# Optimization experiments

Measured on AMD Instinct MI355X. Metric: run time of the kernel, lower is better.

Reference implementation:

```python
import jax, jax.numpy as jnp
import numpy as np

N_QUBITS = 10   # log2(32*32)
N_LAYERS = 5
GRID = 32


def _u3_gates(weights):
    # weights: [L, Q, 3] float32 -> gates: [L, Q, 2, 2] complex64
    th, ph, lm = weights[..., 0], weights[..., 1], weights[..., 2]
    cos = jnp.cos(th / 2)
    sin = jnp.sin(th / 2)
    u00 = cos.astype(jnp.complex64)
    u01 = -jnp.exp(1j * lm) * sin
    u10 = jnp.exp(1j * ph) * sin
    u11 = jnp.exp(1j * (ph + lm)) * cos
    row0 = jnp.stack([u00, u01], axis=-1)
    row1 = jnp.stack([u10, u11], axis=-1)
    return jnp.stack([row0, row1], axis=-2)


def _build_unitary(weights):
    N = 1 << N_QUBITS
    gates = _u3_gates(weights)
    # U as tensor [N, 2, 2, ..., 2]; axis q+1 is qubit q's column index
    U = jnp.eye(N, dtype=jnp.complex64).reshape((N,) + (2,) * N_QUBITS)
    for l in range(N_LAYERS):
        # single-qubit U3 rotations
        for q in range(N_QUBITS):
            ax = q + 1
            s = jnp.moveaxis(U, ax, -1)
            s = jnp.einsum('...a,ba->...b', s, gates[l, q])
            U = jnp.moveaxis(s, -1, ax)
        # circular CNOTs: control q -> target (q+1) % N_QUBITS
        for q in range(N_QUBITS):
            c_ax = q + 1
            t_ax = ((q + 1) % N_QUBITS) + 1
            s = jnp.moveaxis(U, (c_ax, t_ax), (-2, -1))
            # when control bit == 1, flip target bit (swap the two target slices)
            s = s.at[..., 1, :].set(s[..., 1, ::-1])
            U = jnp.moveaxis(s, (-2, -1), (c_ax, t_ax))
    return U.reshape(N, N)


def setup_inputs() -> dict:
    key = jax.random.key(0)
    k1, k2 = jax.random.split(key)
    x_freq = jax.random.normal(k1, (128, 16, GRID, GRID), dtype=jnp.float32)
    weights = jax.random.normal(k2, (N_LAYERS, N_QUBITS, 3), dtype=jnp.float32) * 0.1
    return {"x_freq": x_freq, "weights": weights}


def reference(x_freq, weights):
    B, C, H, W = x_freq.shape
    state = x_freq.reshape(B, C, -1).astype(jnp.complex64)  # [B, C, N]
    U = _build_unitary(weights)                              # [N, N]
    out = jnp.einsum('ij,bcj->bci', U, state)
    return out.reshape(B, C, H, W)
```

## Files before the change

kernel.cpp:

```cpp
#include <hip/hip_runtime.h>


#define NQ 10
#define NL 5
#define NST 1024
#define NTH 64

typedef float f2 __attribute__((ext_vector_type(2)));

constexpr int csigma(int i) {
  for (int q = 0; q < NQ; ++q) {
    const int cb = 9 - q, tb = 9 - ((q + 1) % NQ);
    i ^= ((i >> cb) & 1) << tb;
  }
  return i;
}

__device__ __forceinline__ int swz(int k) { return k ^ (((k >> 4) & 7) << 1); }

__global__ void build_gates(const float* __restrict__ w, float* __restrict__ gw) {
  const int t = threadIdx.x;
  if (t < NL * NQ) {
    const float th = w[t * 3 + 0], ph = w[t * 3 + 1], lm = w[t * 3 + 2];
    const float ch = cosf(0.5f * th), sh = sinf(0.5f * th);
    const float cl = cosf(lm), sl = sinf(lm);
    const float cp = cosf(ph), sp = sinf(ph);
    const float cpl = cosf(ph + lm), spl = sinf(ph + lm);
    float* G = gw + t * 8;
    G[0] = ch;       G[1] = 0.0f;
    G[2] = cp * sh;  G[3] = sp * sh;
    G[4] = -cl * sh; G[5] = -sl * sh;
    G[6] = cpl * ch; G[7] = spl * ch;
  }
}

__device__ __forceinline__ void bfly(f2& a, f2& b, const float h00,
                                     const float h01x, const float h01y,
                                     const float h10x, const float h10y,
                                     const float h11x, const float h11y) {
  const f2 ia = (f2){-a.y, a.x};
  const f2 ib = (f2){-b.y, b.x};
  const f2 na = h00 * a + h01x * b + h01y * ib;
  const f2 nb = h10x * a + h10y * ia + h11x * b + h11y * ib;
  a = na;
  b = nb;
}

#define LOAD_G(G)                                             \
  const float h00 = (G)[0];                                   \
  const float h01x = (G)[2], h01y = (G)[3];                   \
  const float h10x = (G)[4], h10y = (G)[5];                   \
  const float h11x = (G)[6], h11y = (G)[7];

__global__ __launch_bounds__(NTH) void qc_apply(
    const float* __restrict__ x, const float* __restrict__ gw,
    float* __restrict__ out, int out_size) {
  __shared__ alignas(16) f2 sc[NST];

  const int t = threadIdx.x;
  const int sv = blockIdx.x;
  const int m = (t & 7) << 1;

  {
    const float* xs = x + (size_t)sv * NST;
#pragma unroll
    for (int jp = 0; jp < 4; ++jp) {
      const float4 xv = ((const float4*)xs)[t * 4 + jp];
      const int j0 = (jp * 4) ^ m;
      *(float4*)&sc[(t << 4) | j0]       = make_float4(xv.x, 0.f, xv.y, 0.f);
      *(float4*)&sc[(t << 4) | (j0 ^ 2)] = make_float4(xv.z, 0.f, xv.w, 0.f);
    }
  }
  __syncthreads();

  int sL = t;
#pragma unroll
  for (int q = 0; q < NQ; ++q) {
    const int cb = 9 - q, tb = 9 - ((q + 1) % NQ);
    sL ^= ((sL >> cb) & 1) << tb;
  }
  constexpr int SH6 = csigma(1 << 6), SH7 = csigma(1 << 7),
                SH8 = csigma(1 << 8), SH9 = csigma(1 << 9);

  f2 v[16];

#pragma unroll 1
  for (int l = NL - 1; l >= 0; --l) {
    const float* gl = gw + l * NQ * 8;

#pragma unroll
    for (int r = 0; r < 16; ++r) {
      const int idx = sL ^ ((r & 1) ? SH6 : 0) ^ ((r & 2) ? SH7 : 0) ^
                      ((r & 4) ? SH8 : 0) ^ ((r & 8) ? SH9 : 0);
      v[r] = sc[swz(idx)];
    }
#pragma unroll
    for (int e = 0; e < 4; ++e) {
      LOAD_G(gl + (3 - e) * 8)
#pragma unroll
      for (int r = 0; r < 16; ++r)
        if (!(r & (1 << e)))
          bfly(v[r], v[r | (1 << e)], h00, h01x, h01y, h10x, h10y, h11x, h11y);
    }
    __syncthreads();
#pragma unroll
    for (int r = 0; r < 16; ++r) sc[swz((r << 6) | t)] = v[r];
    __syncthreads();

    const int cbase = ((t >> 4) << 8) | (t & 15);
#pragma unroll
    for (int r = 0; r < 16; ++r) v[r] = sc[swz(cbase | (r << 4))];
#pragma unroll
    for (int e = 0; e < 2; ++e) {
      LOAD_G(gl + (5 - e) * 8)
#pragma unroll
      for (int r = 0; r < 16; ++r)
        if (!(r & (1 << e)))
          bfly(v[r], v[r | (1 << e)], h00, h01x, h01y, h10x, h10y, h11x, h11y);
    }
    __syncthreads();
#pragma unroll
    for (int r = 0; r < 16; ++r) sc[swz(cbase | (r << 4))] = v[r];
    __syncthreads();

#pragma unroll
    for (int rp = 0; rp < 8; ++rp) {
      const float4 p = *(const float4*)&sc[(t << 4) | ((2 * rp) ^ m)];
      v[2 * rp]     = (f2){p.x, p.y};
      v[2 * rp + 1] = (f2){p.z, p.w};
    }
#pragma unroll
    for (int e = 0; e < 4; ++e) {
      LOAD_G(gl + (9 - e) * 8)
#pragma unroll
      for (int r = 0; r < 16; ++r)
        if (!(r & (1 << e)))
          bfly(v[r], v[r | (1 << e)], h00, h01x, h01y, h10x, h10y, h11x, h11y);
    }
    if (l != 0) {
#pragma unroll
      for (int rp = 0; rp < 8; ++rp) {
        *(float4*)&sc[(t << 4) | ((2 * rp) ^ m)] =
            make_float4(v[2 * rp].x, v[2 * rp].y,
                        v[2 * rp + 1].x, v[2 * rp + 1].y);
      }
      __syncthreads();
    }
  }

  const size_t ob = (size_t)sv * NST + (t << 4);
#pragma unroll
  for (int rp = 0; rp < 4; ++rp) {
    if (ob + 4 * rp + 4 <= (size_t)out_size)
      *(float4*)(out + ob + 4 * rp) =
          make_float4(v[4 * rp].x, v[4 * rp + 1].x,
                      v[4 * rp + 2].x, v[4 * rp + 3].x);
  }
}

extern "C" void kernel_launch(void* const* d_in, const int* in_sizes, int n_in,
                              void* d_out, int out_size, void* d_ws, size_t ws_size,
                              hipStream_t stream) {
  const float* x = (const float*)d_in[0];
  const float* w = (const float*)d_in[1];
  float* out = (float*)d_out;
  float* gw = (float*)d_ws;
  const int nstates = in_sizes[0] / NST;
  build_gates<<<1, 64, 0, stream>>>(w, gw);
  qc_apply<<<nstates, NTH, 0, stream>>>(x, gw, out, out_size);
}
```

Before: 85.01 us.

## Use 128 threads per state with 8 amplitudes each and shuffle for one qubit

Doubles the threads per state-vector block from 64 to 128, so each thread holds 8 amplitudes instead of 16. The qubit passes are regrouped into three 3-qubit register passes. The tenth qubit (gate index 5) is handled with a cross-lane xor-2 shuffle instead of another shared-memory round trip, which removes one LDS exchange and its barriers per layer. The LDS swizzle is redefined to avoid bank conflicts under the new access patterns. The aim is higher occupancy and latency hiding with lower register pressure, in exchange for more threads and shuffle traffic.

```diff
diff --git a/kernel.cpp b/kernel.cpp
--- a/kernel.cpp
+++ b/kernel.cpp
@@ -4,7 +4,7 @@
 #define NQ 10
 #define NL 5
 #define NST 1024
-#define NTH 64
+#define NTH 128
 
 typedef float f2 __attribute__((ext_vector_type(2)));
 
@@ -16,7 +16,9 @@
   return i;
 }
 
-__device__ __forceinline__ int swz(int k) { return k ^ (((k >> 4) & 7) << 1); }
+__device__ __forceinline__ int swz(int k) {
+  return k ^ ((((k >> 4) ^ (k >> 7)) & 7) << 1);
+}
 
 __global__ void build_gates(const float* __restrict__ w, float* __restrict__ gw) {
   const int t = threadIdx.x;
@@ -59,17 +61,16 @@
 
   const int t = threadIdx.x;
   const int sv = blockIdx.x;
-  const int m = (t & 7) << 1;
+  const int mT = (((t >> 1) ^ (t >> 4)) & 7) << 1;
 
   {
     const float* xs = x + (size_t)sv * NST;
-#pragma unroll
-    for (int jp = 0; jp < 4; ++jp) {
-      const float4 xv = ((const float4*)xs)[t * 4 + jp];
-      const int j0 = (jp * 4) ^ m;
-      *(float4*)&sc[(t << 4) | j0]       = make_float4(xv.x, 0.f, xv.y, 0.f);
-      *(float4*)&sc[(t << 4) | (j0 ^ 2)] = make_float4(xv.z, 0.f, xv.w, 0.f);
-    }
+    const float4 x0 = ((const float4*)xs)[2 * t];
+    const float4 x1 = ((const float4*)xs)[2 * t + 1];
+    *(float4*)&sc[(8 * t + 0) ^ mT] = make_float4(x0.x, 0.f, x0.y, 0.f);
+    *(float4*)&sc[(8 * t + 2) ^ mT] = make_float4(x0.z, 0.f, x0.w, 0.f);
+    *(float4*)&sc[(8 * t + 4) ^ mT] = make_float4(x1.x, 0.f, x1.y, 0.f);
+    *(float4*)&sc[(8 * t + 6) ^ mT] = make_float4(x1.z, 0.f, x1.w, 0.f);
   }
   __syncthreads();
 
@@ -79,82 +80,104 @@
     const int cb = 9 - q, tb = 9 - ((q + 1) % NQ);
     sL ^= ((sL >> cb) & 1) << tb;
   }
-  constexpr int SH6 = csigma(1 << 6), SH7 = csigma(1 << 7),
-                SH8 = csigma(1 << 8), SH9 = csigma(1 << 9);
+  constexpr int SH7 = csigma(1 << 7), SH8 = csigma(1 << 8),
+                SH9 = csigma(1 << 9);
 
-  f2 v[16];
+  f2 v[8];
 
 #pragma unroll 1
   for (int l = NL - 1; l >= 0; --l) {
     const float* gl = gw + l * NQ * 8;
 
 #pragma unroll
-    for (int r = 0; r < 16; ++r) {
-      const int idx = sL ^ ((r & 1) ? SH6 : 0) ^ ((r & 2) ? SH7 : 0) ^
-                      ((r & 4) ? SH8 : 0) ^ ((r & 8) ? SH9 : 0);
+    for (int r = 0; r < 8; ++r) {
+      const int idx = sL ^ ((r & 1) ? SH7 : 0) ^ ((r & 2) ? SH8 : 0) ^
+                      ((r & 4) ? SH9 : 0);
       v[r] = sc[swz(idx)];
     }
 #pragma unroll
-    for (int e = 0; e < 4; ++e) {
-      LOAD_G(gl + (3 - e) * 8)
+    for (int e = 0; e < 3; ++e) {
+      LOAD_G(gl + (2 - e) * 8)
 #pragma unroll
-      for (int r = 0; r < 16; ++r)
+      for (int r = 0; r < 8; ++r)
         if (!(r & (1 << e)))
           bfly(v[r], v[r | (1 << e)], h00, h01x, h01y, h10x, h10y, h11x, h11y);
     }
     __syncthreads();
 #pragma unroll
-    for (int r = 0; r < 16; ++r) sc[swz((r << 6) | t)] = v[r];
+    for (int r = 0; r < 8; ++r) sc[swz((r << 7) | t)] = v[r];
     __syncthreads();
 
-    const int cbase = ((t >> 4) << 8) | (t & 15);
+    const int bbase = (t & 7) | (((t >> 3) & 1) << 4) | ((t >> 4) << 7);
 #pragma unroll
-    for (int r = 0; r < 16; ++r) v[r] = sc[swz(cbase | (r << 4))];
+    for (int r = 0; r < 8; ++r) {
+      const int idx = bbase | ((r & 1) << 3) | (((r >> 1) & 1) << 5) |
+                      (((r >> 2) & 1) << 6);
+      v[r] = sc[swz(idx)];
+    }
+    {
+      const int GQ[3] = {6, 4, 3};
 #pragma unroll
-    for (int e = 0; e < 2; ++e) {
-      LOAD_G(gl + (5 - e) * 8)
+      for (int e = 0; e < 3; ++e) {
+        LOAD_G(gl + GQ[e] * 8)
 #pragma unroll
-      for (int r = 0; r < 16; ++r)
+        for (int r = 0; r < 8; ++r)
+          if (!(r & (1 << e)))
+            bfly(v[r], v[r | (1 << e)], h00, h01x, h01y, h10x, h10y, h11x, h11y);
+      }
+    }
+#pragma unroll
+    for (int r = 0; r < 8; ++r) {
+      const int idx = bbase | ((r & 1) << 3) | (((r >> 1) & 1) << 5) |
+                      (((r >> 2) & 1) << 6);
+      sc[swz(idx)] = v[r];
+    }
+    __syncthreads();
+
+#pragma unroll
+    for (int j0 = 0; j0 < 8; j0 += 2) {
+      const float4 p = *(const float4*)&sc[(8 * t + j0) ^ mT];
+      v[j0]     = (f2){p.x, p.y};
+      v[j0 + 1] = (f2){p.z, p.w};
+    }
+#pragma unroll
+    for (int e = 0; e < 3; ++e) {
+      LOAD_G(gl + (9 - e) * 8)
+#pragma unroll
+      for (int r = 0; r < 8; ++r)
         if (!(r & (1 << e)))
           bfly(v[r], v[r | (1 << e)], h00, h01x, h01y, h10x, h10y, h11x, h11y);
     }
-    __syncthreads();
+    {
+      LOAD_G(gl + 5 * 8)
+      const bool hi = (t >> 1) & 1;
+      const float c1 = hi ? h11x : h00;
+      const float c2 = hi ? h11y : 0.0f;
+      const float c3 = hi ? h10x : h01x;
+      const float c4 = hi ? h10y : h01y;
 #pragma unroll
-    for (int r = 0; r < 16; ++r) sc[swz(cbase | (r << 4))] = v[r];
-    __syncthreads();
-
-#pragma unroll
-    for (int rp = 0; rp < 8; ++rp) {
-      const float4 p = *(const float4*)&sc[(t << 4) | ((2 * rp) ^ m)];
-      v[2 * rp]     = (f2){p.x, p.y};
-      v[2 * rp + 1] = (f2){p.z, p.w};
-    }
-#pragma unroll
-    for (int e = 0; e < 4; ++e) {
-      LOAD_G(gl + (9 - e) * 8)
-#pragma unroll
-      for (int r = 0; r < 16; ++r)
-        if (!(r & (1 << e)))
-          bfly(v[r], v[r | (1 << e)], h00, h01x, h01y, h10x, h10y, h11x, h11y);
+      for (int r = 0; r < 8; ++r) {
+        f2 p;
+        p.x = __shfl_xor(v[r].x, 2);
+        p.y = __shfl_xor(v[r].y, 2);
+        const f2 iv = (f2){-v[r].y, v[r].x};
+        const f2 ip = (f2){-p.y, p.x};
+        v[r] = c1 * v[r] + c2 * iv + c3 * p + c4 * ip;
+      }
     }
     if (l != 0) {
 #pragma unroll
-      for (int rp = 0; rp < 8; ++rp) {
-        *(float4*)&sc[(t << 4) | ((2 * rp) ^ m)] =
-            make_float4(v[2 * rp].x, v[2 * rp].y,
-                        v[2 * rp + 1].x, v[2 * rp + 1].y);
-      }
+      for (int j0 = 0; j0 < 8; j0 += 2)
+        *(float4*)&sc[(8 * t + j0) ^ mT] =
+            make_float4(v[j0].x, v[j0].y, v[j0 + 1].x, v[j0 + 1].y);
       __syncthreads();
     }
   }
 
-  const size_t ob = (size_t)sv * NST + (t << 4);
-#pragma unroll
-  for (int rp = 0; rp < 4; ++rp) {
-    if (ob + 4 * rp + 4 <= (size_t)out_size)
-      *(float4*)(out + ob + 4 * rp) =
-          make_float4(v[4 * rp].x, v[4 * rp + 1].x,
-                      v[4 * rp + 2].x, v[4 * rp + 3].x);
+  const size_t ob = (size_t)sv * NST + 8 * t;
+  if (ob + 8 <= (size_t)out_size) {
+    *(float4*)(out + ob)     = make_float4(v[0].x, v[1].x, v[2].x, v[3].x);
+    *(float4*)(out + ob + 4) = make_float4(v[4].x, v[5].x, v[6].x, v[7].x);
   }
 }
 
```

New measurement: 85.33 us. Within noise of the previous version (+0.4%).

## Rebalance qubit passes to 4/4/2 with new shared-memory layout and swizzle

Applied to the files above, without the earlier changes.

Reorganizes the per-layer qubit grouping so the three shared-memory passes handle 4, 4 and 2 qubits instead of 4, 2 and 4. It introduces a permuted storage layout (rawA) and a new XOR swizzle with precomputed read offsets, so that the permuted reads and writes avoid bank conflicts. The output write is also reshaped so each thread stores coalesced float4 chunks spread across four 256-element segments. The outer layer loop is no longer forced to stay rolled, and the final pass now adds an extra barrier before writing back. The vectorized float4 shared-memory accesses are replaced by scalar f2 ones.

```diff
diff --git a/kernel.cpp b/kernel.cpp
--- a/kernel.cpp
+++ b/kernel.cpp
@@ -16,7 +16,18 @@
   return i;
 }
 
-__device__ __forceinline__ int swz(int k) { return k ^ (((k >> 4) & 7) << 1); }
+constexpr int cswz(int p) { return p ^ ((((p >> 4) ^ (p >> 7)) & 7) << 1); }
+constexpr int crawA(int j) {
+  return (((j >> 2) & 63) << 4) | (j & 3) | (((j >> 8) & 3) << 2);
+}
+constexpr int SRv(int r) { return cswz(crawA(csigma(r << 6))); }
+
+__device__ __forceinline__ int swz(int p) {
+  return p ^ ((((p >> 4) ^ (p >> 7)) & 7) << 1);
+}
+__device__ __forceinline__ int rawA(int j) {
+  return (((j >> 2) & 63) << 4) | (j & 3) | (((j >> 8) & 3) << 2);
+}
 
 __global__ void build_gates(const float* __restrict__ w, float* __restrict__ gw) {
   const int t = threadIdx.x;
@@ -59,41 +70,45 @@
 
   const int t = threadIdx.x;
   const int sv = blockIdx.x;
-  const int m = (t & 7) << 1;
 
   {
     const float* xs = x + (size_t)sv * NST;
 #pragma unroll
-    for (int jp = 0; jp < 4; ++jp) {
-      const float4 xv = ((const float4*)xs)[t * 4 + jp];
-      const int j0 = (jp * 4) ^ m;
-      *(float4*)&sc[(t << 4) | j0]       = make_float4(xv.x, 0.f, xv.y, 0.f);
-      *(float4*)&sc[(t << 4) | (j0 ^ 2)] = make_float4(xv.z, 0.f, xv.w, 0.f);
+    for (int i4 = 0; i4 < 4; ++i4) {
+      const float4 xv = ((const float4*)xs)[4 * t + i4];
+      const int k = 16 * t + 4 * i4;
+      const int pa = swz(rawA(k));
+      *(float4*)&sc[pa]     = make_float4(xv.x, 0.f, xv.y, 0.f);
+      *(float4*)&sc[pa ^ 2] = make_float4(xv.z, 0.f, xv.w, 0.f);
     }
   }
   __syncthreads();
 
-  int sL = t;
+  int st = t;
 #pragma unroll
   for (int q = 0; q < NQ; ++q) {
     const int cb = 9 - q, tb = 9 - ((q + 1) % NQ);
-    sL ^= ((sL >> cb) & 1) << tb;
+    st ^= ((st >> cb) & 1) << tb;
   }
-  constexpr int SH6 = csigma(1 << 6), SH7 = csigma(1 << 7),
-                SH8 = csigma(1 << 8), SH9 = csigma(1 << 9);
+  const int A0 = swz(rawA(st));
+  static constexpr int SR[16] = {
+      SRv(0),  SRv(1),  SRv(2),  SRv(3),  SRv(4),  SRv(5),  SRv(6),  SRv(7),
+      SRv(8),  SRv(9),  SRv(10), SRv(11), SRv(12), SRv(13), SRv(14), SRv(15)};
+
+  const int WB = ((t & 3) << 4) | ((t >> 2) & 15);
+  const int RB = (((t >> 2) & 15) << 6) | ((t & 3) << 4);
+  const int j69 = (t >> 2) & 15;
+  const int WC = ((j69 & 3) << 8) | (t & 3) | (((j69 >> 2) & 3) << 2);
+  const int RC = (((t >> 4) & 3) << 8) | ((t & 15) << 4);
+  const int WA = t << 4;
 
   f2 v[16];
 
-#pragma unroll 1
   for (int l = NL - 1; l >= 0; --l) {
     const float* gl = gw + l * NQ * 8;
 
 #pragma unroll
-    for (int r = 0; r < 16; ++r) {
-      const int idx = sL ^ ((r & 1) ? SH6 : 0) ^ ((r & 2) ? SH7 : 0) ^
-                      ((r & 4) ? SH8 : 0) ^ ((r & 8) ? SH9 : 0);
-      v[r] = sc[swz(idx)];
-    }
+    for (int r = 0; r < 16; ++r) v[r] = sc[A0 ^ SR[r]];
 #pragma unroll
     for (int e = 0; e < 4; ++e) {
       LOAD_G(gl + (3 - e) * 8)
@@ -104,15 +119,14 @@
     }
     __syncthreads();
 #pragma unroll
-    for (int r = 0; r < 16; ++r) sc[swz((r << 6) | t)] = v[r];
+    for (int r = 0; r < 16; ++r) sc[swz(WB | (r << 6))] = v[r];
     __syncthreads();
 
-    const int cbase = ((t >> 4) << 8) | (t & 15);
 #pragma unroll
-    for (int r = 0; r < 16; ++r) v[r] = sc[swz(cbase | (r << 4))];
+    for (int r = 0; r < 16; ++r) v[r] = sc[swz(RB | r)];
 #pragma unroll
-    for (int e = 0; e < 2; ++e) {
-      LOAD_G(gl + (5 - e) * 8)
+    for (int e = 0; e < 4; ++e) {
+      LOAD_G(gl + (7 - e) * 8)
 #pragma unroll
       for (int r = 0; r < 16; ++r)
         if (!(r & (1 << e)))
@@ -120,41 +134,40 @@
     }
     __syncthreads();
 #pragma unroll
-    for (int r = 0; r < 16; ++r) sc[swz(cbase | (r << 4))] = v[r];
+    for (int r = 0; r < 16; ++r) sc[swz(WC | (r << 4))] = v[r];
     __syncthreads();
 
 #pragma unroll
-    for (int rp = 0; rp < 8; ++rp) {
-      const float4 p = *(const float4*)&sc[(t << 4) | ((2 * rp) ^ m)];
-      v[2 * rp]     = (f2){p.x, p.y};
-      v[2 * rp + 1] = (f2){p.z, p.w};
-    }
-#pragma unroll
-    for (int e = 0; e < 4; ++e) {
-      LOAD_G(gl + (9 - e) * 8)
+    for (int r = 0; r < 16; ++r) v[r] = sc[swz(RC | r)];
+    {
+      LOAD_G(gl + 9 * 8)
 #pragma unroll
       for (int r = 0; r < 16; ++r)
-        if (!(r & (1 << e)))
-          bfly(v[r], v[r | (1 << e)], h00, h01x, h01y, h10x, h10y, h11x, h11y);
+        if (!(r & 1))
+          bfly(v[r], v[r | 1], h00, h01x, h01y, h10x, h10y, h11x, h11y);
+    }
+    {
+      LOAD_G(gl + 8 * 8)
+#pragma unroll
+      for (int r = 0; r < 16; ++r)
+        if (!(r & 2))
+          bfly(v[r], v[r | 2], h00, h01x, h01y, h10x, h10y, h11x, h11y);
     }
     if (l != 0) {
+      __syncthreads();
 #pragma unroll
-      for (int rp = 0; rp < 8; ++rp) {
-        *(float4*)&sc[(t << 4) | ((2 * rp) ^ m)] =
-            make_float4(v[2 * rp].x, v[2 * rp].y,
-                        v[2 * rp + 1].x, v[2 * rp + 1].y);
-      }
+      for (int r = 0; r < 16; ++r) sc[swz(WA | r)] = v[r];
       __syncthreads();
     }
   }
 
-  const size_t ob = (size_t)sv * NST + (t << 4);
+  const size_t ob = (size_t)sv * NST;
 #pragma unroll
-  for (int rp = 0; rp < 4; ++rp) {
-    if (ob + 4 * rp + 4 <= (size_t)out_size)
-      *(float4*)(out + ob + 4 * rp) =
-          make_float4(v[4 * rp].x, v[4 * rp + 1].x,
-                      v[4 * rp + 2].x, v[4 * rp + 3].x);
+  for (int h = 0; h < 4; ++h) {
+    const size_t o = ob + (size_t)(h << 8) + (t << 2);
+    if (o + 4 <= (size_t)out_size)
+      *(float4*)(out + o) = make_float4(v[4 * h].x, v[4 * h + 1].x,
+                                        v[4 * h + 2].x, v[4 * h + 3].x);
   }
 }
 
```

Result: no change. 84.36 us (-0.8%).
